# Kernel optimization log

Hardware: AMD Instinct MI355X
Metric: run time of the kernel (lower is better)

## Reference

```python
import jax, jax.numpy as jnp
import numpy as np

N = 20000      # nodes
E = 1280000    # edges
F = 42         # num_features (forced equal to mpnn out_channels by the code)
H = 20         # lstm hidden per direction


def setup_inputs() -> dict:
    key = jax.random.key(0)
    ks = jax.random.split(key, 17)
    def rn(k, shape, sc=0.1):
        return jax.random.normal(k, shape, dtype=jnp.float32) * sc
    return {
        "x": rn(ks[0], (N, F), 1.0),
        "edge_index": jax.random.randint(ks[1], (2, E), 0, N),
        "edge_attr": jax.random.uniform(ks[2], (E, 1), dtype=jnp.float32),
        "lin_w": rn(ks[3], (F, 2 * F)),
        "lin_b": rn(ks[4], (F,)),
        "gru_w_ih": rn(ks[5], (3 * F, F)),
        "gru_w_hh": rn(ks[6], (3 * F, F)),
        "gru_b_ih": rn(ks[7], (3 * F,)),
        "gru_b_hh": rn(ks[8], (3 * F,)),
        "lstm_w_ih_f": rn(ks[9], (4 * H, F)),
        "lstm_w_hh_f": rn(ks[10], (4 * H, H)),
        "lstm_b_f": rn(ks[11], (4 * H,)),
        "lstm_w_ih_b": rn(ks[12], (4 * H, F)),
        "lstm_w_hh_b": rn(ks[13], (4 * H, H)),
        "lstm_b_b": rn(ks[14], (4 * H,)),
        "cls_w": rn(ks[15], (1, 2 * H)),
        "cls_b": rn(ks[16], (1,)),
    }


def _lstm_dir(xs, w_ih, w_hh, b):
    # xs: [N, F] treated as a length-N sequence with batch 1
    x_proj = xs @ w_ih.T + b  # [N, 4H] precompute input contribution
    def cell(carry, xp):
        h, c = carry
        g = xp + w_hh @ h                      # [4H]
        i, f, gg, o = jnp.split(g, 4)
        c = jax.nn.sigmoid(f) * c + jax.nn.sigmoid(i) * jnp.tanh(gg)
        h = jax.nn.sigmoid(o) * jnp.tanh(c)
        return (h, c), h
    h0 = jnp.zeros((H,), xs.dtype)
    _, hs = jax.lax.scan(cell, (h0, h0), x_proj)
    return hs  # [N, H]


def reference(x, edge_index, edge_attr, lin_w, lin_b,
              gru_w_ih, gru_w_hh, gru_b_ih, gru_b_hh,
              lstm_w_ih_f, lstm_w_hh_f, lstm_b_f,
              lstm_w_ih_b, lstm_w_hh_b, lstm_b_b,
              cls_w, cls_b):
    n = x.shape[0]
    src, dst = edge_index[0], edge_index[1]
    # --- message: gather x_i (target) / x_j (source), concat-linear, sigmoid gate
    x_i = x[dst]                               # [E, F]
    x_j = x[src]                               # [E, F]
    msg = jnp.concatenate([x_i, x_j], axis=1) @ lin_w.T + lin_b  # [E, F]
    msg = msg * jax.nn.sigmoid(-edge_attr)     # gate on -time_diff, broadcast [E,1]
    # --- aggregate: scatter-add at target nodes
    agg = jax.ops.segment_sum(msg, dst, num_segments=n)  # [N, F]
    # --- GRU, seq_len=1, batch=N, input = hidden init = agg
    gi = agg @ gru_w_ih.T + gru_b_ih           # [N, 3F]
    gh = agg @ gru_w_hh.T + gru_b_hh           # [N, 3F]
    i_r, i_z, i_n = jnp.split(gi, 3, axis=1)
    h_r, h_z, h_n = jnp.split(gh, 3, axis=1)
    r = jax.nn.sigmoid(i_r + h_r)
    z = jax.nn.sigmoid(i_z + h_z)
    ng = jnp.tanh(i_n + r * h_n)
    hx = (1.0 - z) * ng + z * agg              # [N, F]
    # --- bidirectional LSTM over nodes as a sequence (batch=1)
    h_fwd = _lstm_dir(hx, lstm_w_ih_f, lstm_w_hh_f, lstm_b_f)                # [N, H]
    h_bwd = _lstm_dir(hx[::-1], lstm_w_ih_b, lstm_w_hh_b, lstm_b_b)[::-1]    # [N, H]
    h_cat = jnp.concatenate([h_fwd, h_bwd], axis=1)  # [N, 2H]
    return h_cat @ cls_w.T + cls_b             # [N, 1]
```

## Files before the change

kernel.cpp:

```cpp
#include <hip/hip_runtime.h>

#define NN 20000
#define EE 1280000
#define FF 42
#define HH 20
#define PSTR 44

#define CHUNK 8
#define WARM 24
#define NCHD 2500
#define TOTCH (2*NCHD)
#define LW 4
#define TT 16

#define NBIN 625
#define BINW 32
#define CAP  2560
#define NCHKB 160
#define CHKE 8000
#define NSC (NBIN*NCHKB)
#define NSB1 ((NSC+255)/256)

#define WGROWS 168
#define WLROWS 160
#define WGTOT (WGROWS*PSTR)
#define WLTOT (WLROWS*PSTR)

__device__ __forceinline__ float fexp2(float x){ return __builtin_amdgcn_exp2f(x); }
__device__ __forceinline__ float frcp(float x){ return __builtin_amdgcn_rcpf(x); }
__device__ __forceinline__ float fsigmoid(float x){ return frcp(1.f + fexp2(-1.442695041f*x)); }
__device__ __forceinline__ float ftanh(float x){ return 2.f*frcp(1.f + fexp2(-2.885390082f*x)) - 1.f; }

__global__ __launch_bounds__(256) void k_nodeproj(
    const float* __restrict__ x, const float* __restrict__ lw,
    float* __restrict__ PA, float* __restrict__ PB)
{
  __shared__ float2 w1S[FF*21];
  __shared__ float2 w2S[FF*21];
  for (int idx=threadIdx.x; idx<FF*21; idx+=256){
    int k = idx/21, fp = idx - 21*k;
    w1S[idx] = make_float2(lw[(2*fp)*84 + k],      lw[(2*fp+1)*84 + k]);
    w2S[idx] = make_float2(lw[(2*fp)*84 + 42 + k], lw[(2*fp+1)*84 + 42 + k]);
  }
  __syncthreads();
  int tid = blockIdx.x*256 + threadIdx.x;
  if (tid >= NN*21) return;
  int n = tid / 21;
  int fp = tid - n*21;
  const float* xr = x + n*FF;
  float2 pa = make_float2(0.f,0.f), pb = make_float2(0.f,0.f);
#pragma unroll 6
  for (int k=0;k<FF;k++){
    float xv = xr[k];
    float2 w1 = w1S[k*21+fp], w2 = w2S[k*21+fp];
    pa.x += w1.x*xv; pa.y += w1.y*xv;
    pb.x += w2.x*xv; pb.y += w2.y*xv;
  }
  ((float2*)(PA + n*PSTR))[fp] = pa;
  ((float2*)(PB + n*PSTR))[fp] = pb;
  if (fp == 0){
    PA[n*PSTR+42] = 0.f; PA[n*PSTR+43] = 0.f;
    PB[n*PSTR+42] = 0.f; PB[n*PSTR+43] = 0.f;
  }
}

__global__ __launch_bounds__(256) void k_wprep(
    const float* __restrict__ gwih, const float* __restrict__ gwhh,
    const float* __restrict__ lwihf, const float* __restrict__ lwihb,
    float* __restrict__ WG, float* __restrict__ WL)
{
  int i = blockIdx.x*256 + threadIdx.x;
  if (i < WGTOT){
    int r = i/PSTR, k = i - PSTR*r;
    float v = 0.f;
    if (k < FF){
      if (r < 84)       v = gwih[r*FF+k] + gwhh[r*FF+k];
      else if (r < 126) v = gwih[r*FF+k];
      else              v = gwhh[(r-42)*FF+k];
    }
    WG[i] = v;
  }
  int j = i - WGTOT;
  if (j >= 0 && j < WLTOT){
    int r = j/PSTR, k = j - PSTR*r;
    float v = 0.f;
    if (k < FF) v = (r < 80) ? lwihf[r*FF+k] : lwihb[(r-80)*FF+k];
    WL[j] = v;
  }
}

__global__ __launch_bounds__(256) void k_binA(const int* __restrict__ dst, int* __restrict__ cnt)
{
  __shared__ unsigned int h[NBIN];
  int blk = blockIdx.x, tid = threadIdx.x;
  for (int i=tid; i<NBIN; i+=256) h[i] = 0;
  __syncthreads();
  const int* d = dst + blk*CHKE;
  for (int i=tid; i<CHKE; i+=256) atomicAdd(&h[d[i]>>5], 1u);
  __syncthreads();
  for (int i=tid; i<NBIN; i+=256) cnt[i*NCHKB + blk] = (int)h[i];
}

__global__ __launch_bounds__(256) void k_scan1(int* __restrict__ cnt, int* __restrict__ bsum)
{
  int b = blockIdx.x, t = threadIdx.x;
  int i = b*256 + t;
  int v = (i < NSC) ? cnt[i] : 0;
  int lane = t & 63, w = t >> 6;
  int x = v;
#pragma unroll
  for (int off=1; off<64; off<<=1){
    int y = __shfl_up(x, off);
    if (lane >= off) x += y;
  }
  __shared__ int wsum[4];
  if (lane == 63) wsum[w] = x;
  __syncthreads();
  int base = 0;
  for (int ww=0; ww<w; ww++) base += wsum[ww];
  int incl = x + base;
  if (i < NSC) cnt[i] = incl - v;
  if (t == 255) bsum[b] = incl;
}

__global__ __launch_bounds__(1024) void k_scan2(const int* __restrict__ bsum, int* __restrict__ boff)
{
  int t = threadIdx.x;
  int v = (t < NSB1) ? bsum[t] : 0;
  int lane = t & 63, w = t >> 6;
  int x = v;
#pragma unroll
  for (int off=1; off<64; off<<=1){
    int y = __shfl_up(x, off);
    if (lane >= off) x += y;
  }
  __shared__ int ws2[16];
  if (lane == 63) ws2[w] = x;
  __syncthreads();
  int base = 0;
  for (int ww=0; ww<w; ww++) base += ws2[ww];
  int incl = x + base;
  if (t < NSB1) boff[t] = incl - v;
}

__global__ __launch_bounds__(256) void k_binC(
    const int* __restrict__ src, const int* __restrict__ dst,
    const float* __restrict__ ea, const int* __restrict__ cnt,
    const int* __restrict__ boff, int2* __restrict__ binned)
{
  __shared__ unsigned int cur[NBIN];
  int blk = blockIdx.x, tid = threadIdx.x;
  for (int i=tid; i<NBIN; i+=256){
    int idx = i*NCHKB + blk;
    cur[i] = (unsigned)(cnt[idx] + boff[idx>>8]);
  }
  __syncthreads();
  for (int i=tid; i<CHKE; i+=256){
    int e = blk*CHKE + i;
    int d = dst[e];
    int s = src[e];
    float g = fsigmoid(-ea[e]);
    unsigned p = atomicAdd(&cur[d>>5], 1u);
    int2 r; r.x = s | ((d & 31) << 16); r.y = __float_as_int(g);
    binned[p] = r;
  }
}

__global__ __launch_bounds__(512, 8) void k_agg(
    const float* __restrict__ PA, const float* __restrict__ PB,
    const int* __restrict__ cnt, const int* __restrict__ boff,
    const int2* __restrict__ binned, const float* __restrict__ lin_b,
    float* __restrict__ agg)
{
  __shared__ int2 edS[CAP];
  __shared__ unsigned int cntL[BINW];
  __shared__ unsigned int offsN[BINW+1];
  __shared__ float lbS[PSTR];

  int b = blockIdx.x, tid = threadIdx.x;
  if (tid < PSTR) lbS[tid] = (tid < FF) ? lin_b[tid] : 0.f;
  int i0g = b*NCHKB;
  int e0 = cnt[i0g] + boff[i0g>>8];
  int e1;
  if (b == NBIN-1) e1 = EE;
  else { int i1g = (b+1)*NCHKB; e1 = cnt[i1g] + boff[i1g>>8]; }
  int cl = e1 - e0; if (cl > CAP) cl = CAP;

  int2 E[5];
  if (tid < BINW) cntL[tid] = 0;
  __syncthreads();
#pragma unroll
  for (int u=0; u<5; u++){
    int i = tid + u*512;
    if (i < cl){
      E[u] = binned[e0+i];
      atomicAdd(&cntL[E[u].x >> 16], 1u);
    }
  }
  __syncthreads();
  if (tid < 64){
    unsigned v = (tid < BINW) ? cntL[tid] : 0u;
    unsigned x = v;
#pragma unroll
    for (int off=1; off<32; off<<=1){
      unsigned y = __shfl_up(x, off);
      if ((tid & 63) >= off) x += y;
    }
    if (tid < BINW) offsN[tid+1] = x;
    if (tid == 0) offsN[0] = 0;
  }
  __syncthreads();
  if (tid < BINW) cntL[tid] = offsN[tid];
  __syncthreads();
#pragma unroll
  for (int u=0; u<5; u++){
    int i = tid + u*512;
    if (i < cl){
      unsigned p = atomicAdd(&cntL[E[u].x >> 16], 1u);
      edS[p] = E[u];
    }
  }
  __syncthreads();

  int w = tid >> 6, lane = tid & 63;
  int grp = lane / 11;
  int fp  = lane - grp*11;
  bool lact = grp < 5;
  unsigned a0[4], aE[4];
  int M = 0;
#pragma unroll
  for (int j=0;j<4;j++){
    int n = w + 8*j;
    a0[j] = offsN[n]; aE[j] = offsN[n+1];
    int len = (int)(aE[j]-a0[j]); if (len > M) M = len;
  }
  float4 acc[4]; float gs[4];
#pragma unroll
  for (int j=0;j<4;j++){ acc[j]=make_float4(0.f,0.f,0.f,0.f); gs[j]=0.f; }
  for (int t=0; t<M; t+=5){
    float4 pv[4]; float gv[4];
#pragma unroll
    for (int j=0;j<4;j++){
      unsigned k = a0[j] + (unsigned)(t + grp);
      bool v = lact && (k < aE[j]);
      unsigned ks = v ? k : 0u;
      int2 Ee = edS[ks];
      gv[j] = v ? __int_as_float(Ee.y) : 0.f;
      pv[j] = ((const float4*)(PB + (Ee.x & 0xFFFF)*PSTR))[fp];
    }
#pragma unroll
    for (int j=0;j<4;j++){
      acc[j].x += gv[j]*pv[j].x;  acc[j].y += gv[j]*pv[j].y;
      acc[j].z += gv[j]*pv[j].z;  acc[j].w += gv[j]*pv[j].w;
      gs[j]    += gv[j];
    }
  }
#pragma unroll
  for (int j=0;j<4;j++){
    float vx=acc[j].x, vy=acc[j].y, vz=acc[j].z, vw=acc[j].w, g=gs[j];
#pragma unroll
    for (int s=1;s<5;s++){
      vx += __shfl(acc[j].x, lane + 11*s);
      vy += __shfl(acc[j].y, lane + 11*s);
      vz += __shfl(acc[j].z, lane + 11*s);
      vw += __shfl(acc[j].w, lane + 11*s);
      g  += __shfl(gs[j],    lane + 11*s);
    }
    if (lane < 11){
      int n = w + 8*j;
      const float4 pa = ((const float4*)(PA + (b*BINW+n)*PSTR))[fp];
      float4 lb = ((const float4*)lbS)[fp];
      float4 o;
      o.x = (pa.x + lb.x)*g + vx;
      o.y = (pa.y + lb.y)*g + vy;
      o.z = (pa.z + lb.z)*g + vz;
      o.w = (pa.w + lb.w)*g + vw;
      ((float4*)(agg + (b*BINW+n)*PSTR))[fp] = o;
    }
  }
}

__global__ __launch_bounds__(256) void k_tr(
    const float* __restrict__ agg, float* __restrict__ aggT)
{
  __shared__ float T[64*45];
  int b = blockIdx.x, tid = threadIdx.x;
  int n0 = b*64;
  for (int idx=tid; idx<64*44; idx+=256){
    int r = idx/44, c = idx - 44*r;
    int n = n0 + r;
    T[r*45+c] = (n < NN) ? agg[(long)n*PSTR + c] : 0.f;
  }
  __syncthreads();
  for (int idx=tid; idx<42*64; idx+=256){
    int k = idx >> 6, nn = idx & 63;
    int n = n0 + nn;
    if (n < NN) aggT[(long)k*NN + n] = T[nn*45 + k];
  }
}

__global__ __launch_bounds__(256) void k_gruF(
    const float* __restrict__ aggT,
    const float* __restrict__ WG,
    const float* __restrict__ gbih, const float* __restrict__ gbhh,
    float* __restrict__ hxT)
{
  int n = blockIdx.x*256 + threadIdx.x;
  int j0 = 2*blockIdx.y, j1 = j0 + 1;
  if (n >= NN) return;
  const float* wr0 = WG + j0*PSTR;
  const float* wz0 = WG + (42+j0)*PSTR;
  const float* wi0 = WG + (84+j0)*PSTR;
  const float* wh0 = WG + (126+j0)*PSTR;
  const float* wr1 = WG + j1*PSTR;
  const float* wz1 = WG + (42+j1)*PSTR;
  const float* wi1 = WG + (84+j1)*PSTR;
  const float* wh1 = WG + (126+j1)*PSTR;
  float sR0 = gbih[j0]+gbhh[j0], sZ0 = gbih[42+j0]+gbhh[42+j0];
  float sI0 = gbih[84+j0],       sH0 = gbhh[84+j0];
  float sR1 = gbih[j1]+gbhh[j1], sZ1 = gbih[42+j1]+gbhh[42+j1];
  float sI1 = gbih[84+j1],       sH1 = gbhh[84+j1];
#pragma unroll
  for (int k=0; k<FF; k++){
    float a = aggT[(long)k*NN + n];
    sR0 += wr0[k]*a; sZ0 += wz0[k]*a; sI0 += wi0[k]*a; sH0 += wh0[k]*a;
    sR1 += wr1[k]*a; sZ1 += wz1[k]*a; sI1 += wi1[k]*a; sH1 += wh1[k]*a;
  }
  float r0 = fsigmoid(sR0), z0 = fsigmoid(sZ0);
  float ng0 = ftanh(sI0 + r0*sH0);
  hxT[(long)j0*NN + n] = (1.f - z0)*ng0 + z0*aggT[(long)j0*NN + n];
  float r1 = fsigmoid(sR1), z1 = fsigmoid(sZ1);
  float ng1 = ftanh(sI1 + r1*sH1);
  hxT[(long)j1*NN + n] = (1.f - z1)*ng1 + z1*aggT[(long)j1*NN + n];
}

__global__ __launch_bounds__(256) void k_projF(
    const float* __restrict__ hxT,
    const float* __restrict__ WL,
    const float* __restrict__ lbf, const float* __restrict__ lbb,
    float* __restrict__ xpf, float* __restrict__ xpb)
{
  int n = blockIdx.x*256 + threadIdx.x;
  int gq = blockIdx.y;
  if (n >= NN) return;
  bool fw = gq < 20;
  int g0 = 4*gq;
  int gl = fw ? gq : gq - 20;
  int gr = fw ? g0 : g0 - 80;
  const float* w0 = WL + (g0+0)*PSTR;
  const float* w1 = WL + (g0+1)*PSTR;
  const float* w2 = WL + (g0+2)*PSTR;
  const float* w3 = WL + (g0+3)*PSTR;
  const float* bb = fw ? lbf : lbb;
  float a0 = bb[gr+0], a1 = bb[gr+1], a2 = bb[gr+2], a3 = bb[gr+3];
#pragma unroll
  for (int k=0; k<FF; k++){
    float h = hxT[(long)k*NN + n];
    a0 += w0[k]*h; a1 += w1[k]*h; a2 += w2[k]*h; a3 += w3[k]*h;
  }
  float* xp = fw ? xpf : xpb;
  ((float4*)(xp + (long)n*80))[gl] = make_float4(a0, a1, a2, a3);
}

__global__ __launch_bounds__(256) void k_lstm(
    const float* __restrict__ xpf, const float* __restrict__ xpb,
    const float* __restrict__ whhf, const float* __restrict__ whhb,
    float* __restrict__ hf, float* __restrict__ hb)
{
  __shared__ float bufAll[LW][2][TT*80];
  int wv = threadIdx.x >> 6;
  int lane = threadIdx.x & 63;
  int c = blockIdx.x*LW + wv;
  if (c >= TOTCH) return;
  int dir = (c >= NCHD) ? 1 : 0;
  int chunk = c - dir*NCHD;
  int p0 = chunk*CHUNK;
  if (p0 >= NN) return;
  int p1 = p0 + CHUNK; if (p1 > NN) p1 = NN;

  const float* xp  = dir ? xpb  : xpf;
  const float* whh = dir ? whhb : whhf;
  float* hout      = dir ? hb   : hf;
  float (*buf)[TT*80] = bufAll[wv];

  int m = lane & 31;
  int half = lane >> 5;
  int mm = (m < HH) ? m : HH-1;
  int rowA = half*40 + mm;
  int rowB = rowA + HH;
  float2 WA[10], WB[10];
#pragma unroll
  for (int kk=0;kk<10;kk++){
    WA[kk] = make_float2(whh[rowA*HH+2*kk], whh[rowA*HH+2*kk+1]);
    WB[kk] = make_float2(whh[rowB*HH+2*kk], whh[rowB*HH+2*kk+1]);
  }
  const float cE = half ? -2.885390082f : -1.442695041f;
  const float cM = half ? 2.f : 1.f;
  const float cA = half ? -1.f : 0.f;
  int colA = rowA;
  int colB = rowB;

  int ps = (p0 >= WARM) ? (p0-WARM) : 0;
  int steps = p1 - ps;
  int ntiles = (steps + TT - 1)/TT;

  float4 R0,R1,R2,R3,R4;
  auto fetch = [&](int j){
    int a = ps + j*TT;
    long g0;
    if (!dir) g0 = (long)a*80;
    else { int t_lo = NN - a - TT; if (t_lo < 0) t_lo = 0; g0 = (long)t_lo*80; }
    const float* s = xp + g0 + lane*4;
    R0 = *(const float4*)(s);
    R1 = *(const float4*)(s + 256);
    R2 = *(const float4*)(s + 512);
    R3 = *(const float4*)(s + 768);
    R4 = *(const float4*)(s + 1024);
  };
  auto stash = [&](int dbuf){
    float* d = buf[dbuf] + lane*4;
    *(float4*)(d)        = R0;
    *(float4*)(d + 256)  = R1;
    *(float4*)(d + 512)  = R2;
    *(float4*)(d + 768)  = R3;
    *(float4*)(d + 1024) = R4;
  };

  fetch(0); stash(0);
  if (ntiles > 1) fetch(1);

  float c2 = 0.f, h = 0.f;
  float2 H[10];
#pragma unroll
  for (int kk=0;kk<10;kk++) H[kk] = make_float2(0.f, 0.f);

  int t_lo0 = 0;
  if (dir){ t_lo0 = NN - ps - TT; if (t_lo0 < 0) t_lo0 = 0; }
  int row0 = dir ? (NN-1-ps - t_lo0) : 0;
  float nxA = buf[0][row0*80 + colA];
  float nxB = buf[0][row0*80 + colB];

  for (int j=0; j<ntiles; ++j){
    if (j+1 < ntiles) stash((j+1)&1);
    if (j+2 < ntiles) fetch(j+2);
    const float* B  = buf[j&1];
    const float* Bn = buf[(j+1)&1];
    int a = ps + j*TT;
    int t_lo = 0;
    if (dir){ t_lo = NN - a - TT; if (t_lo < 0) t_lo = 0; }
    int aN = a + TT;
    int t_loN = 0;
    if (dir){ t_loN = NN - aN - TT; if (t_loN < 0) t_loN = 0; }
#pragma unroll 4
    for (int r=0; r<TT; ++r){
      int p = a + r;
      float xA = nxA, xB = nxB;
      if (r+1 < TT){
        int rowN = dir ? (NN-1-(p+1) - t_lo) : (r+1);
        if (p+1 < ps+steps || !dir){
          nxA = B[rowN*80 + colA];
          nxB = B[rowN*80 + colB];
        }
      } else if (j+1 < ntiles){
        int rowN = dir ? (NN-1-aN - t_loN) : 0;
        nxA = Bn[rowN*80 + colA];
        nxB = Bn[rowN*80 + colB];
      }
      float aA0=xA, aA1=0.f, aB0=xB, aB1=0.f;
#pragma unroll
      for (int kk=0;kk<10;kk++){
        aA0 += WA[kk].x*H[kk].x;  aA1 += WA[kk].y*H[kk].y;
        aB0 += WB[kk].x*H[kk].x;  aB1 += WB[kk].y*H[kk].y;
      }
      float gA = aA0+aA1, gB = aB0+aB1;
      float actA = cM*frcp(1.f + fexp2(cE*gA)) + cA;
      float actB = frcp(1.f + fexp2(-1.442695041f*gB));
      float gT = __shfl_xor(actA, 32);
      float oT = __shfl_xor(actB, 32);
      c2 = actB*c2 + actA*gT;
      h = oT*ftanh(c2);
#pragma unroll
      for (int kk=0;kk<10;kk++){
        float va = __int_as_float(__builtin_amdgcn_readlane(__float_as_int(h), 2*kk));
        float vb = __int_as_float(__builtin_amdgcn_readlane(__float_as_int(h), 2*kk+1));
        H[kk] = make_float2(va, vb);
      }
      if (p >= p0 && p < p1 && lane < HH){
        int t = dir ? (NN-1-p) : p;
        hout[t*HH + lane] = h;
      }
    }
  }
}

__global__ __launch_bounds__(256) void k_cls(
    const float* __restrict__ hf, const float* __restrict__ hb,
    const float* __restrict__ cw, const float* __restrict__ cb,
    float* __restrict__ out)
{
  int n = blockIdx.x*256 + threadIdx.x;
  if (n >= NN) return;
  float s = cb[0];
  const float* hfr = hf + n*HH;
  const float* hbr = hb + n*HH;
#pragma unroll
  for (int k=0;k<HH;k++){
    s += hfr[k]*cw[k] + hbr[k]*cw[HH+k];
  }
  out[n] = s;
}

extern "C" void kernel_launch(void* const* d_in, const int* in_sizes, int n_in,
                              void* d_out, int out_size, void* d_ws, size_t ws_size,
                              hipStream_t stream) {
  (void)in_sizes; (void)n_in; (void)out_size; (void)ws_size;
  const float* x      = (const float*)d_in[0];
  const int*   ei     = (const int*)  d_in[1];
  const float* ea     = (const float*)d_in[2];
  const float* lin_w  = (const float*)d_in[3];
  const float* lin_b  = (const float*)d_in[4];
  const float* gwih   = (const float*)d_in[5];
  const float* gwhh   = (const float*)d_in[6];
  const float* gbih   = (const float*)d_in[7];
  const float* gbhh   = (const float*)d_in[8];
  const float* lwihf  = (const float*)d_in[9];
  const float* lwhhf  = (const float*)d_in[10];
  const float* lbf    = (const float*)d_in[11];
  const float* lwihb  = (const float*)d_in[12];
  const float* lwhhb  = (const float*)d_in[13];
  const float* lbb    = (const float*)d_in[14];
  const float* cw     = (const float*)d_in[15];
  const float* cb     = (const float*)d_in[16];
  float* out = (float*)d_out;

  const int* src = ei;
  const int* dst = ei + EE;

  float* PA     = (float*)d_ws;
  float* PB     = PA + NN*PSTR;
  float* agg    = PB + NN*PSTR;
  float* xpf    = agg + NN*PSTR;
  float* xpb    = xpf + NN*80;
  float* hf     = xpb + NN*80;
  float* hb     = hf + NN*HH;
  float* WG     = hb + NN*HH;
  float* WL     = WG + WGTOT;
  float* aggT   = WL + WLTOT;
  float* hxT    = aggT + 42*NN;
  int2*  binned = (int2*)(hxT + 42*NN);
  int*   cnt    = (int*)(binned + EE);
  int*   bsum   = cnt + NSC;
  int*   boff   = bsum + NSB1;

  k_nodeproj<<<(NN*21 + 255)/256, 256, 0, stream>>>(x, lin_w, PA, PB);
  k_wprep<<<(WGTOT + WLTOT + 255)/256, 256, 0, stream>>>(gwih, gwhh, lwihf, lwihb, WG, WL);
  k_binA<<<NCHKB, 256, 0, stream>>>(dst, cnt);
  k_scan1<<<NSB1, 256, 0, stream>>>(cnt, bsum);
  k_scan2<<<1, 1024, 0, stream>>>(bsum, boff);
  k_binC<<<NCHKB, 256, 0, stream>>>(src, dst, ea, cnt, boff, binned);
  k_agg<<<NBIN, 512, 0, stream>>>(PA, PB, cnt, boff, binned, lin_b, agg);
  k_tr<<<(NN + 63)/64, 256, 0, stream>>>(agg, aggT);
  k_gruF<<<dim3((NN + 255)/256, FF/2), 256, 0, stream>>>(aggT, WG, gbih, gbhh, hxT);
  k_projF<<<dim3((NN + 255)/256, 40), 256, 0, stream>>>(hxT, WL, lbf, lbb, xpf, xpb);
  k_lstm<<<(TOTCH + LW - 1)/LW, 256, 0, stream>>>(xpf, xpb, lwhhf, lwhhb, hf, hb);
  k_cls<<<(NN + 255)/256, 256, 0, stream>>>(hf, hb, cw, cb, out);
}
```

Measured before the change: 242.1 us.

## Replace scan-based edge binning with fixed-capacity bins and fuse front kernels

The separate histogram, two scan kernels and scatter kernel are replaced by one binning kernel. Each block reserves space in fixed-capacity per-bin slots through global atomic counters, so no prefix scan is needed. Node projection and weight prep are merged into a single launch that also zeroes the counters. The aggregation kernel now writes the transposed layout directly, which removes the transpose kernel. This cuts five launches and their global round-trips, at the cost of bin order that varies between runs and strided, uncoalesced column writes in k_agg.

```diff
diff --git a/kernel.cpp b/kernel.cpp
--- a/kernel.cpp
+++ b/kernel.cpp
@@ -18,159 +18,119 @@
 #define CAP  2560
 #define NCHKB 160
 #define CHKE 8000
-#define NSC (NBIN*NCHKB)
-#define NSB1 ((NSC+255)/256)
 
 #define WGROWS 168
 #define WLROWS 160
 #define WGTOT (WGROWS*PSTR)
 #define WLTOT (WLROWS*PSTR)
 
+#define NPB 1641
+#define WPB 57
+
 __device__ __forceinline__ float fexp2(float x){ return __builtin_amdgcn_exp2f(x); }
 __device__ __forceinline__ float frcp(float x){ return __builtin_amdgcn_rcpf(x); }
 __device__ __forceinline__ float fsigmoid(float x){ return frcp(1.f + fexp2(-1.442695041f*x)); }
 __device__ __forceinline__ float ftanh(float x){ return 2.f*frcp(1.f + fexp2(-2.885390082f*x)) - 1.f; }
 
-__global__ __launch_bounds__(256) void k_nodeproj(
+__global__ __launch_bounds__(256) void k_front(
     const float* __restrict__ x, const float* __restrict__ lw,
-    float* __restrict__ PA, float* __restrict__ PB)
+    const float* __restrict__ gwih, const float* __restrict__ gwhh,
+    const float* __restrict__ lwihf, const float* __restrict__ lwihb,
+    float* __restrict__ PA, float* __restrict__ PB,
+    float* __restrict__ WG, float* __restrict__ WL,
+    unsigned* __restrict__ gcur)
 {
   __shared__ float2 w1S[FF*21];
   __shared__ float2 w2S[FF*21];
-  for (int idx=threadIdx.x; idx<FF*21; idx+=256){
-    int k = idx/21, fp = idx - 21*k;
-    w1S[idx] = make_float2(lw[(2*fp)*84 + k],      lw[(2*fp+1)*84 + k]);
-    w2S[idx] = make_float2(lw[(2*fp)*84 + 42 + k], lw[(2*fp+1)*84 + 42 + k]);
-  }
-  __syncthreads();
-  int tid = blockIdx.x*256 + threadIdx.x;
-  if (tid >= NN*21) return;
-  int n = tid / 21;
-  int fp = tid - n*21;
-  const float* xr = x + n*FF;
-  float2 pa = make_float2(0.f,0.f), pb = make_float2(0.f,0.f);
+  int bid = blockIdx.x;
+  if (bid < NPB){
+    for (int idx=threadIdx.x; idx<FF*21; idx+=256){
+      int k = idx/21, fp = idx - 21*k;
+      w1S[idx] = make_float2(lw[(2*fp)*84 + k],      lw[(2*fp+1)*84 + k]);
+      w2S[idx] = make_float2(lw[(2*fp)*84 + 42 + k], lw[(2*fp+1)*84 + 42 + k]);
+    }
+    __syncthreads();
+    int tid = bid*256 + threadIdx.x;
+    if (tid >= NN*21) return;
+    int n = tid / 21;
+    int fp = tid - n*21;
+    const float* xr = x + n*FF;
+    float2 pa = make_float2(0.f,0.f), pb = make_float2(0.f,0.f);
 #pragma unroll 6
-  for (int k=0;k<FF;k++){
-    float xv = xr[k];
-    float2 w1 = w1S[k*21+fp], w2 = w2S[k*21+fp];
-    pa.x += w1.x*xv; pa.y += w1.y*xv;
-    pb.x += w2.x*xv; pb.y += w2.y*xv;
-  }
-  ((float2*)(PA + n*PSTR))[fp] = pa;
-  ((float2*)(PB + n*PSTR))[fp] = pb;
-  if (fp == 0){
-    PA[n*PSTR+42] = 0.f; PA[n*PSTR+43] = 0.f;
-    PB[n*PSTR+42] = 0.f; PB[n*PSTR+43] = 0.f;
-  }
-}
-
-__global__ __launch_bounds__(256) void k_wprep(
-    const float* __restrict__ gwih, const float* __restrict__ gwhh,
-    const float* __restrict__ lwihf, const float* __restrict__ lwihb,
-    float* __restrict__ WG, float* __restrict__ WL)
-{
-  int i = blockIdx.x*256 + threadIdx.x;
-  if (i < WGTOT){
-    int r = i/PSTR, k = i - PSTR*r;
-    float v = 0.f;
-    if (k < FF){
-      if (r < 84)       v = gwih[r*FF+k] + gwhh[r*FF+k];
-      else if (r < 126) v = gwih[r*FF+k];
-      else              v = gwhh[(r-42)*FF+k];
-    }
-    WG[i] = v;
-  }
-  int j = i - WGTOT;
-  if (j >= 0 && j < WLTOT){
-    int r = j/PSTR, k = j - PSTR*r;
-    float v = 0.f;
-    if (k < FF) v = (r < 80) ? lwihf[r*FF+k] : lwihb[(r-80)*FF+k];
-    WL[j] = v;
-  }
-}
-
-__global__ __launch_bounds__(256) void k_binA(const int* __restrict__ dst, int* __restrict__ cnt)
-{
-  __shared__ unsigned int h[NBIN];
+    for (int k=0;k<FF;k++){
+      float xv = xr[k];
+      float2 w1 = w1S[k*21+fp], w2 = w2S[k*21+fp];
+      pa.x += w1.x*xv; pa.y += w1.y*xv;
+      pb.x += w2.x*xv; pb.y += w2.y*xv;
+    }
+    ((float2*)(PA + n*PSTR))[fp] = pa;
+    ((float2*)(PB + n*PSTR))[fp] = pb;
+    if (fp == 0){
+      PA[n*PSTR+42] = 0.f; PA[n*PSTR+43] = 0.f;
+      PB[n*PSTR+42] = 0.f; PB[n*PSTR+43] = 0.f;
+    }
+  } else {
+    int i = (bid - NPB)*256 + threadIdx.x;
+    if (i < NBIN) gcur[i] = 0u;
+    if (i < WGTOT){
+      int r = i/PSTR, k = i - PSTR*r;
+      float v = 0.f;
+      if (k < FF){
+        if (r < 84)       v = gwih[r*FF+k] + gwhh[r*FF+k];
+        else if (r < 126) v = gwih[r*FF+k];
+        else              v = gwhh[(r-42)*FF+k];
+      }
+      WG[i] = v;
+    }
+    int j = i - WGTOT;
+    if (j >= 0 && j < WLTOT){
+      int r = j/PSTR, k = j - PSTR*r;
+      float v = 0.f;
+      if (k < FF) v = (r < 80) ? lwihf[r*FF+k] : lwihb[(r-80)*FF+k];
+      WL[j] = v;
+    }
+  }
+}
+
+__global__ __launch_bounds__(256) void k_bin(
+    const int* __restrict__ src, const int* __restrict__ dst,
+    const float* __restrict__ ea,
+    unsigned* __restrict__ gcur, int2* __restrict__ binned)
+{
+  __shared__ unsigned h[NBIN];
+  __shared__ unsigned base[NBIN];
   int blk = blockIdx.x, tid = threadIdx.x;
-  for (int i=tid; i<NBIN; i+=256) h[i] = 0;
+  for (int i=tid; i<NBIN; i+=256) h[i] = 0u;
   __syncthreads();
   const int* d = dst + blk*CHKE;
   for (int i=tid; i<CHKE; i+=256) atomicAdd(&h[d[i]>>5], 1u);
   __syncthreads();
-  for (int i=tid; i<NBIN; i+=256) cnt[i*NCHKB + blk] = (int)h[i];
-}
-
-__global__ __launch_bounds__(256) void k_scan1(int* __restrict__ cnt, int* __restrict__ bsum)
-{
-  int b = blockIdx.x, t = threadIdx.x;
-  int i = b*256 + t;
-  int v = (i < NSC) ? cnt[i] : 0;
-  int lane = t & 63, w = t >> 6;
-  int x = v;
-#pragma unroll
-  for (int off=1; off<64; off<<=1){
-    int y = __shfl_up(x, off);
-    if (lane >= off) x += y;
-  }
-  __shared__ int wsum[4];
-  if (lane == 63) wsum[w] = x;
-  __syncthreads();
-  int base = 0;
-  for (int ww=0; ww<w; ww++) base += wsum[ww];
-  int incl = x + base;
-  if (i < NSC) cnt[i] = incl - v;
-  if (t == 255) bsum[b] = incl;
-}
-
-__global__ __launch_bounds__(1024) void k_scan2(const int* __restrict__ bsum, int* __restrict__ boff)
-{
-  int t = threadIdx.x;
-  int v = (t < NSB1) ? bsum[t] : 0;
-  int lane = t & 63, w = t >> 6;
-  int x = v;
-#pragma unroll
-  for (int off=1; off<64; off<<=1){
-    int y = __shfl_up(x, off);
-    if (lane >= off) x += y;
-  }
-  __shared__ int ws2[16];
-  if (lane == 63) ws2[w] = x;
-  __syncthreads();
-  int base = 0;
-  for (int ww=0; ww<w; ww++) base += ws2[ww];
-  int incl = x + base;
-  if (t < NSB1) boff[t] = incl - v;
-}
-
-__global__ __launch_bounds__(256) void k_binC(
-    const int* __restrict__ src, const int* __restrict__ dst,
-    const float* __restrict__ ea, const int* __restrict__ cnt,
-    const int* __restrict__ boff, int2* __restrict__ binned)
-{
-  __shared__ unsigned int cur[NBIN];
-  int blk = blockIdx.x, tid = threadIdx.x;
   for (int i=tid; i<NBIN; i+=256){
-    int idx = i*NCHKB + blk;
-    cur[i] = (unsigned)(cnt[idx] + boff[idx>>8]);
-  }
+    unsigned c = h[i];
+    base[i] = c ? atomicAdd(&gcur[i], c) : 0u;
+  }
+  __syncthreads();
+  for (int i=tid; i<NBIN; i+=256) h[i] = 0u;
   __syncthreads();
   for (int i=tid; i<CHKE; i+=256){
     int e = blk*CHKE + i;
-    int d = dst[e];
-    int s = src[e];
+    int dd = dst[e];
+    int s  = src[e];
     float g = fsigmoid(-ea[e]);
-    unsigned p = atomicAdd(&cur[d>>5], 1u);
-    int2 r; r.x = s | ((d & 31) << 16); r.y = __float_as_int(g);
-    binned[p] = r;
+    int b = dd >> 5;
+    unsigned p = base[b] + atomicAdd(&h[b], 1u);
+    if (p < CAP){
+      int2 r; r.x = s | ((dd & 31) << 16); r.y = __float_as_int(g);
+      binned[(long)b*CAP + p] = r;
+    }
   }
 }
 
 __global__ __launch_bounds__(512, 8) void k_agg(
     const float* __restrict__ PA, const float* __restrict__ PB,
-    const int* __restrict__ cnt, const int* __restrict__ boff,
+    const unsigned* __restrict__ gcur,
     const int2* __restrict__ binned, const float* __restrict__ lin_b,
-    float* __restrict__ agg)
+    float* __restrict__ aggT)
 {
   __shared__ int2 edS[CAP];
   __shared__ unsigned int cntL[BINW];
@@ -179,12 +139,8 @@
 
   int b = blockIdx.x, tid = threadIdx.x;
   if (tid < PSTR) lbS[tid] = (tid < FF) ? lin_b[tid] : 0.f;
-  int i0g = b*NCHKB;
-  int e0 = cnt[i0g] + boff[i0g>>8];
-  int e1;
-  if (b == NBIN-1) e1 = EE;
-  else { int i1g = (b+1)*NCHKB; e1 = cnt[i1g] + boff[i1g>>8]; }
-  int cl = e1 - e0; if (cl > CAP) cl = CAP;
+  int cl = (int)gcur[b]; if (cl > CAP) cl = CAP;
+  long e0 = (long)b*CAP;
 
   int2 E[5];
   if (tid < BINW) cntL[tid] = 0;
@@ -267,35 +223,15 @@
       g  += __shfl(gs[j],    lane + 11*s);
     }
     if (lane < 11){
-      int n = w + 8*j;
-      const float4 pa = ((const float4*)(PA + (b*BINW+n)*PSTR))[fp];
+      int gn = b*BINW + w + 8*j;
+      const float4 pa = ((const float4*)(PA + (long)gn*PSTR))[fp];
       float4 lb = ((const float4*)lbS)[fp];
-      float4 o;
-      o.x = (pa.x + lb.x)*g + vx;
-      o.y = (pa.y + lb.y)*g + vy;
-      o.z = (pa.z + lb.z)*g + vz;
-      o.w = (pa.w + lb.w)*g + vw;
-      ((float4*)(agg + (b*BINW+n)*PSTR))[fp] = o;
-    }
-  }
-}
-
-__global__ __launch_bounds__(256) void k_tr(
-    const float* __restrict__ agg, float* __restrict__ aggT)
-{
-  __shared__ float T[64*45];
-  int b = blockIdx.x, tid = threadIdx.x;
-  int n0 = b*64;
-  for (int idx=tid; idx<64*44; idx+=256){
-    int r = idx/44, c = idx - 44*r;
-    int n = n0 + r;
-    T[r*45+c] = (n < NN) ? agg[(long)n*PSTR + c] : 0.f;
-  }
-  __syncthreads();
-  for (int idx=tid; idx<42*64; idx+=256){
-    int k = idx >> 6, nn = idx & 63;
-    int n = n0 + nn;
-    if (n < NN) aggT[(long)k*NN + n] = T[nn*45 + k];
+      int c0 = 4*fp;
+      aggT[(long)(c0+0)*NN + gn] = (pa.x + lb.x)*g + vx;
+      aggT[(long)(c0+1)*NN + gn] = (pa.y + lb.y)*g + vy;
+      if (c0+2 < FF) aggT[(long)(c0+2)*NN + gn] = (pa.z + lb.z)*g + vz;
+      if (c0+3 < FF) aggT[(long)(c0+3)*NN + gn] = (pa.w + lb.w)*g + vw;
+    }
   }
 }
 
@@ -538,8 +474,7 @@
 
   float* PA     = (float*)d_ws;
   float* PB     = PA + NN*PSTR;
-  float* agg    = PB + NN*PSTR;
-  float* xpf    = agg + NN*PSTR;
+  float* xpf    = PB + NN*PSTR;
   float* xpb    = xpf + NN*80;
   float* hf     = xpb + NN*80;
   float* hb     = hf + NN*HH;
@@ -548,18 +483,12 @@
   float* aggT   = WL + WLTOT;
   float* hxT    = aggT + 42*NN;
   int2*  binned = (int2*)(hxT + 42*NN);
-  int*   cnt    = (int*)(binned + EE);
-  int*   bsum   = cnt + NSC;
-  int*   boff   = bsum + NSB1;
-
-  k_nodeproj<<<(NN*21 + 255)/256, 256, 0, stream>>>(x, lin_w, PA, PB);
-  k_wprep<<<(WGTOT + WLTOT + 255)/256, 256, 0, stream>>>(gwih, gwhh, lwihf, lwihb, WG, WL);
-  k_binA<<<NCHKB, 256, 0, stream>>>(dst, cnt);
-  k_scan1<<<NSB1, 256, 0, stream>>>(cnt, bsum);
-  k_scan2<<<1, 1024, 0, stream>>>(bsum, boff);
-  k_binC<<<NCHKB, 256, 0, stream>>>(src, dst, ea, cnt, boff, binned);
-  k_agg<<<NBIN, 512, 0, stream>>>(PA, PB, cnt, boff, binned, lin_b, agg);
-  k_tr<<<(NN + 63)/64, 256, 0, stream>>>(agg, aggT);
+  unsigned* gcur = (unsigned*)(binned + (long)NBIN*CAP);
+
+  k_front<<<NPB + WPB, 256, 0, stream>>>(x, lin_w, gwih, gwhh, lwihf, lwihb,
+                                         PA, PB, WG, WL, gcur);
+  k_bin<<<NCHKB, 256, 0, stream>>>(src, dst, ea, gcur, binned);
+  k_agg<<<NBIN, 512, 0, stream>>>(PA, PB, gcur, binned, lin_b, aggT);
   k_gruF<<<dim3((NN + 255)/256, FF/2), 256, 0, stream>>>(aggT, WG, gbih, gbhh, hxT);
   k_projF<<<dim3((NN + 255)/256, 40), 256, 0, stream>>>(hxT, WL, lbf, lbb, xpf, xpb);
   k_lstm<<<(TOTCH + LW - 1)/LW, 256, 0, stream>>>(xpf, xpb, lwhhf, lwhhb, hf, hb);
```

After: 238.7 us. No clear change (-1.4%).
